# Optimization experiments

Measured on AMD Instinct MI355X. Metric: run time of the kernel, lower is better.

## Reference

```python
import jax, jax.numpy as jnp
import numpy as np
from jax import lax

NUM_EXPERTS = 256
TOP_K = 8
HIDDEN = 7168
N_GROUP = 8
TOPK_GROUP = 4
SCALING = 2.5
NORM_TOPK = True
EPG = NUM_EXPERTS // N_GROUP  # experts per group = 32


def setup_inputs() -> dict:
    key = jax.random.key(0)
    k1, k2, k3 = jax.random.split(key, 3)
    hidden_states = jax.random.normal(k1, (4, 2048, HIDDEN), dtype=jnp.float32)
    weight = jax.random.normal(k2, (NUM_EXPERTS, HIDDEN), dtype=jnp.float32) * 0.02
    e_score_correction_bias = jax.random.normal(k3, (NUM_EXPERTS,), dtype=jnp.float32) * 0.1
    return {"hidden_states": hidden_states, "weight": weight,
            "e_score_correction_bias": e_score_correction_bias}


def reference(hidden_states, weight, e_score_correction_bias):
    x = hidden_states.reshape(-1, hidden_states.shape[-1]).astype(jnp.float32)  # [T, H]
    router_logits = jnp.einsum('th,eh->te', x, weight.astype(jnp.float32))       # [T, E]
    scores = jax.nn.sigmoid(router_logits)
    scores_for_choice = scores + e_score_correction_bias[None, :]
    grouped = scores_for_choice.reshape(-1, N_GROUP, EPG)                        # [T, G, epg]
    group_scores = grouped.sum(axis=-1)                                          # [T, G]
    _, group_idx = lax.top_k(group_scores, TOPK_GROUP)                            # [T, kg]
    selected = jnp.take_along_axis(grouped, group_idx[:, :, None], axis=1)        # [T, kg, epg]
    flat = selected.reshape(-1, TOPK_GROUP * EPG)                                 # [T, kg*epg]
    _, flat_idx = lax.top_k(flat, TOP_K)                                          # [T, K]
    group_ord = flat_idx // EPG
    within = flat_idx % EPG
    actual_group = jnp.take_along_axis(group_idx, group_ord, axis=1)
    topk_indices = actual_group * EPG + within                                    # [T, K]
    topk_weights = jnp.take_along_axis(scores, topk_indices, axis=1)              # [T, K]
    if NORM_TOPK:
        topk_weights = topk_weights / (topk_weights.sum(axis=-1, keepdims=True) + 1e-20)
    topk_weights = topk_weights * SCALING
    return topk_indices, topk_weights
```

## Files before the change

### kernel.cpp

```cpp
#include <hip/hip_runtime.h>
#include <float.h>
#include <math.h>

#define NUM_T 8192
#define NUM_E 256
#define HID   7168

typedef __attribute__((ext_vector_type(16))) float f32x16;
typedef __attribute__((ext_vector_type(4))) _Float16 f16x4;
typedef __attribute__((ext_vector_type(8))) _Float16 f16x8;

#define MFMA(a, b, c) __builtin_amdgcn_mfma_f32_32x32x16_f16(a, b, c, 0, 0, 0)

__device__ __forceinline__ int lds_off(int row, int c8) {
  return (row << 6) + ((c8 ^ (row & 15)) << 2);
}

__device__ __forceinline__ void cvt4(float4 v, f16x4& h, f16x4& l) {
  h[0] = (_Float16)v.x; h[1] = (_Float16)v.y;
  h[2] = (_Float16)v.z; h[3] = (_Float16)v.w;
  l[0] = (_Float16)(v.x - (float)h[0]);
  l[1] = (_Float16)(v.y - (float)h[1]);
  l[2] = (_Float16)(v.z - (float)h[2]);
  l[3] = (_Float16)(v.w - (float)h[3]);
}

__device__ __forceinline__ f16x8 frag(const _Float16* buf, int row, int c8) {
  const f16x4 p0 = *reinterpret_cast<const f16x4*>(buf + lds_off(row, c8));
  const f16x4 p1 = *reinterpret_cast<const f16x4*>(buf + lds_off(row, c8 + 1));
  return __builtin_shufflevector(p0, p1, 0, 1, 2, 3, 4, 5, 6, 7);
}

template <int S>
__global__ __launch_bounds__(512, 2) void router_gemm_mfma(
    const float* __restrict__ X, const float* __restrict__ W,
    float* __restrict__ partial) {
  __shared__ _Float16 smem[2][384 * 64];

  const int tid = threadIdx.x;
  const int bid = blockIdx.x;
  int bx, by;
  if (S == 4) {
    const int xcd = bid & 7;
    by = xcd >> 1;
    bx = (bid >> 3) * 2 + (xcd & 1);
  } else if (S == 2) {
    const int xcd = bid & 7;
    by = xcd >> 2;
    bx = (bid >> 3) * 4 + (xcd & 3);
  } else {
    by = 0;
    bx = bid;
  }

  const int kLen = HID / S;
  const int nch = kLen / 32;
  const int t0 = bx * 128;
  const int k0 = by * kLen;

  const int xr = tid >> 2, xq = tid & 3;
  const int wr = tid >> 1, wq = tid & 1;
  const float* Xp = X + (size_t)(t0 + xr) * HID + k0 + xq * 8;
  const float* Wp = W + (size_t)wr * HID + k0 + wq * 16;

  int xo[4], wo[8];
  xo[0] = lds_off(xr, xq * 2);
  xo[1] = lds_off(xr, xq * 2 + 1);
  xo[2] = lds_off(xr, 8 + xq * 2);
  xo[3] = lds_off(xr, 8 + xq * 2 + 1);
#pragma unroll
  for (int j = 0; j < 4; ++j) {
    wo[j] = lds_off(128 + wr, wq * 4 + j);
    wo[4 + j] = lds_off(128 + wr, 8 + wq * 4 + j);
  }

  const int l = tid & 63, wave = tid >> 6;
  const int wm = wave >> 2, wn = wave & 3;
  const int la = l & 31, kh = l >> 5;
  const int ar0 = wm * 64 + la;
  const int br0 = 128 + wn * 64 + la;

  f32x16 acc[2][2];
#pragma unroll
  for (int i = 0; i < 2; ++i)
#pragma unroll
    for (int j = 0; j < 2; ++j)
#pragma unroll
      for (int r = 0; r < 16; ++r) acc[i][j][r] = 0.f;

  float4 xv[2], wv[4];

#define LOADC()                                            \
  do {                                                     \
    xv[0] = *reinterpret_cast<const float4*>(Xp);          \
    xv[1] = *reinterpret_cast<const float4*>(Xp + 4);      \
    wv[0] = *reinterpret_cast<const float4*>(Wp);          \
    wv[1] = *reinterpret_cast<const float4*>(Wp + 4);      \
    wv[2] = *reinterpret_cast<const float4*>(Wp + 8);      \
    wv[3] = *reinterpret_cast<const float4*>(Wp + 12);     \
    Xp += 32;                                              \
    Wp += 32;                                              \
  } while (0)

#define STAGE(dst)                                         \
  do {                                                     \
    f16x4 h_, l_;                                          \
    cvt4(xv[0], h_, l_);                                   \
    *reinterpret_cast<f16x4*>((dst) + xo[0]) = h_;         \
    *reinterpret_cast<f16x4*>((dst) + xo[2]) = l_;         \
    cvt4(xv[1], h_, l_);                                   \
    *reinterpret_cast<f16x4*>((dst) + xo[1]) = h_;         \
    *reinterpret_cast<f16x4*>((dst) + xo[3]) = l_;         \
    _Pragma("unroll") for (int j = 0; j < 4; ++j) {        \
      cvt4(wv[j], h_, l_);                                 \
      *reinterpret_cast<f16x4*>((dst) + wo[j]) = h_;       \
      *reinterpret_cast<f16x4*>((dst) + wo[4 + j]) = l_;   \
    }                                                      \
  } while (0)

  LOADC();
  STAGE(&smem[0][0]);
  __syncthreads();

  int cur = 0;
  for (int c = 0; c < nch; ++c) {
    const bool more = (c + 1) < nch;
    if (more) LOADC();

    const _Float16* buf = &smem[cur][0];
#pragma unroll
    for (int ks = 0; ks < 2; ++ks) {
      const int cb = ks * 4 + kh * 2;
      f16x8 ah0 = frag(buf, ar0, cb);
      f16x8 ah1 = frag(buf, ar0 + 32, cb);
      f16x8 bh0 = frag(buf, br0, cb);
      f16x8 bh1 = frag(buf, br0 + 32, cb);
      f16x8 al0 = frag(buf, ar0, cb + 8);
      f16x8 al1 = frag(buf, ar0 + 32, cb + 8);
      f16x8 bl0 = frag(buf, br0, cb + 8);
      f16x8 bl1 = frag(buf, br0 + 32, cb + 8);
      acc[0][0] = MFMA(ah0, bh0, acc[0][0]);
      acc[0][1] = MFMA(ah0, bh1, acc[0][1]);
      acc[1][0] = MFMA(ah1, bh0, acc[1][0]);
      acc[1][1] = MFMA(ah1, bh1, acc[1][1]);
      acc[0][0] = MFMA(ah0, bl0, acc[0][0]);
      acc[0][1] = MFMA(ah0, bl1, acc[0][1]);
      acc[1][0] = MFMA(ah1, bl0, acc[1][0]);
      acc[1][1] = MFMA(ah1, bl1, acc[1][1]);
      acc[0][0] = MFMA(al0, bh0, acc[0][0]);
      acc[0][1] = MFMA(al0, bh1, acc[0][1]);
      acc[1][0] = MFMA(al1, bh0, acc[1][0]);
      acc[1][1] = MFMA(al1, bh1, acc[1][1]);
    }

    if (more) STAGE(&smem[cur ^ 1][0]);
    __syncthreads();
    cur ^= 1;
  }

  float* out = partial + (size_t)by * NUM_T * NUM_E;
#pragma unroll
  for (int ti = 0; ti < 2; ++ti)
#pragma unroll
    for (int tj = 0; tj < 2; ++tj) {
      const int col = wn * 64 + tj * 32 + la;
      const int rb = t0 + wm * 64 + ti * 32 + 4 * kh;
#pragma unroll
      for (int r = 0; r < 16; ++r) {
        const int row = rb + (r & 3) + 8 * (r >> 2);
        out[(size_t)row * NUM_E + col] = acc[ti][tj][r];
      }
    }
#undef LOADC
#undef STAGE
}

__global__ __launch_bounds__(256) void router_select(
    const float* __restrict__ partial, int splitk,
    const float* __restrict__ bias, float* __restrict__ outIdx,
    float* __restrict__ outW) {
  const int lane = threadIdx.x & 63;
  const int t = blockIdx.x * 4 + (threadIdx.x >> 6);

  float lg[4] = {0.f, 0.f, 0.f, 0.f};
  for (int s = 0; s < splitk; ++s) {
    const float4 p = *reinterpret_cast<const float4*>(
        partial + ((size_t)s * NUM_T + t) * NUM_E + lane * 4);
    lg[0] += p.x;
    lg[1] += p.y;
    lg[2] += p.z;
    lg[3] += p.w;
  }
  const float4 bv = *reinterpret_cast<const float4*>(bias + lane * 4);

  float sc[4], bs[4];
#pragma unroll
  for (int j = 0; j < 4; ++j) {
    sc[j] = 1.0f / (1.0f + expf(-lg[j]));
  }
  bs[0] = sc[0] + bv.x;
  bs[1] = sc[1] + bv.y;
  bs[2] = sc[2] + bv.z;
  bs[3] = sc[3] + bv.w;

  const int myg = lane >> 3;
  float gsum = bs[0] + bs[1] + bs[2] + bs[3];
#pragma unroll
  for (int d = 1; d < 8; d <<= 1) gsum += __shfl_xor(gsum, d);

  float gsv[8];
#pragma unroll
  for (int g = 0; g < 8; ++g) gsv[g] = __shfl(gsum, g * 8);

  unsigned selm = 0;
  int myrank = 0;
#pragma unroll
  for (int r = 0; r < 4; ++r) {
    int best = -1;
    float bvv = -FLT_MAX;
#pragma unroll
    for (int g = 0; g < 8; ++g) {
      if (!((selm >> g) & 1u) && gsv[g] > bvv) {
        bvv = gsv[g];
        best = g;
      }
    }
    selm |= 1u << best;
    if (best == myg) myrank = r;
  }
  const bool gsel = ((selm >> myg) & 1u) != 0u;

  float myv[4];
#pragma unroll
  for (int j = 0; j < 4; ++j) myv[j] = gsel ? bs[j] : -FLT_MAX;

  const int ebase = lane << 2;
  const int flatb = myrank * 32 + (lane & 7) * 4;

  float chosen_s = 0.f;
  int ex_out = 0;
  float ssum = 0.f;
  for (int r = 0; r < 8; ++r) {
    float v = -FLT_MAX;
    int fl = 1 << 30;
    int ex = 0;
    float s = 0.f;
#pragma unroll
    for (int j = 0; j < 4; ++j) {
      const bool better = (myv[j] > v) || (myv[j] == v && (flatb + j) < fl);
      if (better) {
        v = myv[j];
        fl = flatb + j;
        ex = ebase + j;
        s = sc[j];
      }
    }
#pragma unroll
    for (int d = 32; d > 0; d >>= 1) {
      const float v2 = __shfl_xor(v, d);
      const int fl2 = __shfl_xor(fl, d);
      const int ex2 = __shfl_xor(ex, d);
      const float s2 = __shfl_xor(s, d);
      if (v2 > v || (v2 == v && fl2 < fl)) {
        v = v2;
        fl = fl2;
        ex = ex2;
        s = s2;
      }
    }
    ssum += s;
    if (lane == r) {
      chosen_s = s;
      ex_out = ex;
    }
    if ((ex >> 2) == lane) myv[ex & 3] = -FLT_MAX;
  }

  if (lane < 8) {
    outIdx[t * 8 + lane] = (float)ex_out;
    outW[t * 8 + lane] = chosen_s / (ssum + 1e-20f) * 2.5f;
  }
}

extern "C" void kernel_launch(void* const* d_in, const int* in_sizes, int n_in,
                              void* d_out, int out_size, void* d_ws,
                              size_t ws_size, hipStream_t stream) {
  const float* X = (const float*)d_in[0];
  const float* W = (const float*)d_in[1];
  const float* bias = (const float*)d_in[2];
  float* partial = (float*)d_ws;

  const size_t slice = (size_t)NUM_T * NUM_E * sizeof(float);
  int S;
  if (ws_size >= 4 * slice)
    S = 4;
  else if (ws_size >= 2 * slice)
    S = 2;
  else
    S = 1;

  if (S == 4)
    router_gemm_mfma<4><<<dim3(64 * 4), dim3(512), 0, stream>>>(X, W, partial);
  else if (S == 2)
    router_gemm_mfma<2><<<dim3(64 * 2), dim3(512), 0, stream>>>(X, W, partial);
  else
    router_gemm_mfma<1><<<dim3(64), dim3(512), 0, stream>>>(X, W, partial);

  float* outIdx = (float*)d_out;
  float* outW = outIdx + NUM_T * 8;
  router_select<<<NUM_T / 4, 256, 0, stream>>>(partial, S, bias, outIdx, outW);
}
```

Before: 441.7 us.

## Pad LDS rows, unroll main loop by two with deeper register prefetch

Replaces the XOR-swizzled LDS layout with padded rows of 136 bytes and precomputed byte pointers, which simplifies address arithmetic. The main loop is unrolled by two with two register staging sets, so global loads run two chunks ahead. __syncthreads is replaced with an explicit lgkmcnt wait plus s_barrier. The goal is to hide global load latency and cut index math, at the cost of extra VGPRs for the second staging set and possible bank conflicts from the padded layout. The loop now assumes an even chunk count.

```diff
diff --git a/kernel.cpp b/kernel.cpp
--- a/kernel.cpp
+++ b/kernel.cpp
@@ -6,15 +6,16 @@
 #define NUM_E 256
 #define HID   7168
 
+#define ROWB 136
+#define BUFB (384 * ROWB)
+
 typedef __attribute__((ext_vector_type(16))) float f32x16;
 typedef __attribute__((ext_vector_type(4))) _Float16 f16x4;
 typedef __attribute__((ext_vector_type(8))) _Float16 f16x8;
 
 #define MFMA(a, b, c) __builtin_amdgcn_mfma_f32_32x32x16_f16(a, b, c, 0, 0, 0)
 
-__device__ __forceinline__ int lds_off(int row, int c8) {
-  return (row << 6) + ((c8 ^ (row & 15)) << 2);
-}
+#define BARRIER() asm volatile("s_waitcnt lgkmcnt(0)\n\ts_barrier" ::: "memory")
 
 __device__ __forceinline__ void cvt4(float4 v, f16x4& h, f16x4& l) {
   h[0] = (_Float16)v.x; h[1] = (_Float16)v.y;
@@ -25,17 +26,21 @@
   l[3] = (_Float16)(v.w - (float)h[3]);
 }
 
-__device__ __forceinline__ f16x8 frag(const _Float16* buf, int row, int c8) {
-  const f16x4 p0 = *reinterpret_cast<const f16x4*>(buf + lds_off(row, c8));
-  const f16x4 p1 = *reinterpret_cast<const f16x4*>(buf + lds_off(row, c8 + 1));
-  return __builtin_shufflevector(p0, p1, 0, 1, 2, 3, 4, 5, 6, 7);
-}
+__device__ __forceinline__ f16x8 fr(const char* p, int off) {
+  const f16x4 a = *reinterpret_cast<const f16x4*>(p + off);
+  const f16x4 b = *reinterpret_cast<const f16x4*>(p + off + 8);
+  return __builtin_shufflevector(a, b, 0, 1, 2, 3, 4, 5, 6, 7);
+}
+
+struct Q {
+  float4 x0, x1, w0, w1, w2, w3;
+};
 
 template <int S>
 __global__ __launch_bounds__(512, 2) void router_gemm_mfma(
     const float* __restrict__ X, const float* __restrict__ W,
     float* __restrict__ partial) {
-  __shared__ _Float16 smem[2][384 * 64];
+  __shared__ __align__(16) char lds[2 * BUFB];
 
   const int tid = threadIdx.x;
   const int bid = blockIdx.x;
@@ -62,23 +67,14 @@
   const int wr = tid >> 1, wq = tid & 1;
   const float* Xp = X + (size_t)(t0 + xr) * HID + k0 + xq * 8;
   const float* Wp = W + (size_t)wr * HID + k0 + wq * 16;
-
-  int xo[4], wo[8];
-  xo[0] = lds_off(xr, xq * 2);
-  xo[1] = lds_off(xr, xq * 2 + 1);
-  xo[2] = lds_off(xr, 8 + xq * 2);
-  xo[3] = lds_off(xr, 8 + xq * 2 + 1);
-#pragma unroll
-  for (int j = 0; j < 4; ++j) {
-    wo[j] = lds_off(128 + wr, wq * 4 + j);
-    wo[4 + j] = lds_off(128 + wr, 8 + wq * 4 + j);
-  }
+  char* wx = lds + xr * ROWB + xq * 16;
+  char* ww = lds + (128 + wr) * ROWB + wq * 32;
 
   const int l = tid & 63, wave = tid >> 6;
   const int wm = wave >> 2, wn = wave & 3;
   const int la = l & 31, kh = l >> 5;
-  const int ar0 = wm * 64 + la;
-  const int br0 = 128 + wn * 64 + la;
+  const char* ra = lds + (wm * 64 + la) * ROWB + kh * 16;
+  const char* rb = lds + (128 + wn * 64 + la) * ROWB + kh * 16;
 
   f32x16 acc[2][2];
 #pragma unroll
@@ -88,74 +84,83 @@
 #pragma unroll
       for (int r = 0; r < 16; ++r) acc[i][j][r] = 0.f;
 
-  float4 xv[2], wv[4];
-
-#define LOADC()                                            \
-  do {                                                     \
-    xv[0] = *reinterpret_cast<const float4*>(Xp);          \
-    xv[1] = *reinterpret_cast<const float4*>(Xp + 4);      \
-    wv[0] = *reinterpret_cast<const float4*>(Wp);          \
-    wv[1] = *reinterpret_cast<const float4*>(Wp + 4);      \
-    wv[2] = *reinterpret_cast<const float4*>(Wp + 8);      \
-    wv[3] = *reinterpret_cast<const float4*>(Wp + 12);     \
-    Xp += 32;                                              \
-    Wp += 32;                                              \
+#define LOADC(q)                                   \
+  do {                                             \
+    q.x0 = *reinterpret_cast<const float4*>(Xp);   \
+    q.x1 = *reinterpret_cast<const float4*>(Xp + 4); \
+    q.w0 = *reinterpret_cast<const float4*>(Wp);   \
+    q.w1 = *reinterpret_cast<const float4*>(Wp + 4); \
+    q.w2 = *reinterpret_cast<const float4*>(Wp + 8); \
+    q.w3 = *reinterpret_cast<const float4*>(Wp + 12); \
+    Xp += 32;                                      \
+    Wp += 32;                                      \
   } while (0)
 
-#define STAGE(dst)                                         \
-  do {                                                     \
-    f16x4 h_, l_;                                          \
-    cvt4(xv[0], h_, l_);                                   \
-    *reinterpret_cast<f16x4*>((dst) + xo[0]) = h_;         \
-    *reinterpret_cast<f16x4*>((dst) + xo[2]) = l_;         \
-    cvt4(xv[1], h_, l_);                                   \
-    *reinterpret_cast<f16x4*>((dst) + xo[1]) = h_;         \
-    *reinterpret_cast<f16x4*>((dst) + xo[3]) = l_;         \
-    _Pragma("unroll") for (int j = 0; j < 4; ++j) {        \
-      cvt4(wv[j], h_, l_);                                 \
-      *reinterpret_cast<f16x4*>((dst) + wo[j]) = h_;       \
-      *reinterpret_cast<f16x4*>((dst) + wo[4 + j]) = l_;   \
-    }                                                      \
+#define STAGE(B, q)                                            \
+  do {                                                         \
+    f16x4 h_, l_;                                              \
+    cvt4(q.x0, h_, l_);                                        \
+    *reinterpret_cast<f16x4*>(wx + (B) + 0) = h_;              \
+    *reinterpret_cast<f16x4*>(wx + (B) + 64) = l_;             \
+    cvt4(q.x1, h_, l_);                                        \
+    *reinterpret_cast<f16x4*>(wx + (B) + 8) = h_;              \
+    *reinterpret_cast<f16x4*>(wx + (B) + 72) = l_;             \
+    cvt4(q.w0, h_, l_);                                        \
+    *reinterpret_cast<f16x4*>(ww + (B) + 0) = h_;              \
+    *reinterpret_cast<f16x4*>(ww + (B) + 64) = l_;             \
+    cvt4(q.w1, h_, l_);                                        \
+    *reinterpret_cast<f16x4*>(ww + (B) + 8) = h_;              \
+    *reinterpret_cast<f16x4*>(ww + (B) + 72) = l_;             \
+    cvt4(q.w2, h_, l_);                                        \
+    *reinterpret_cast<f16x4*>(ww + (B) + 16) = h_;             \
+    *reinterpret_cast<f16x4*>(ww + (B) + 80) = l_;             \
+    cvt4(q.w3, h_, l_);                                        \
+    *reinterpret_cast<f16x4*>(ww + (B) + 24) = h_;             \
+    *reinterpret_cast<f16x4*>(ww + (B) + 88) = l_;             \
   } while (0)
 
-  LOADC();
-  STAGE(&smem[0][0]);
-  __syncthreads();
-
-  int cur = 0;
-  for (int c = 0; c < nch; ++c) {
-    const bool more = (c + 1) < nch;
-    if (more) LOADC();
-
-    const _Float16* buf = &smem[cur][0];
-#pragma unroll
-    for (int ks = 0; ks < 2; ++ks) {
-      const int cb = ks * 4 + kh * 2;
-      f16x8 ah0 = frag(buf, ar0, cb);
-      f16x8 ah1 = frag(buf, ar0 + 32, cb);
-      f16x8 bh0 = frag(buf, br0, cb);
-      f16x8 bh1 = frag(buf, br0 + 32, cb);
-      f16x8 al0 = frag(buf, ar0, cb + 8);
-      f16x8 al1 = frag(buf, ar0 + 32, cb + 8);
-      f16x8 bl0 = frag(buf, br0, cb + 8);
-      f16x8 bl1 = frag(buf, br0 + 32, cb + 8);
-      acc[0][0] = MFMA(ah0, bh0, acc[0][0]);
-      acc[0][1] = MFMA(ah0, bh1, acc[0][1]);
-      acc[1][0] = MFMA(ah1, bh0, acc[1][0]);
-      acc[1][1] = MFMA(ah1, bh1, acc[1][1]);
-      acc[0][0] = MFMA(ah0, bl0, acc[0][0]);
-      acc[0][1] = MFMA(ah0, bl1, acc[0][1]);
-      acc[1][0] = MFMA(ah1, bl0, acc[1][0]);
-      acc[1][1] = MFMA(ah1, bl1, acc[1][1]);
-      acc[0][0] = MFMA(al0, bh0, acc[0][0]);
-      acc[0][1] = MFMA(al0, bh1, acc[0][1]);
-      acc[1][0] = MFMA(al1, bh0, acc[1][0]);
-      acc[1][1] = MFMA(al1, bh1, acc[1][1]);
-    }
-
-    if (more) STAGE(&smem[cur ^ 1][0]);
-    __syncthreads();
-    cur ^= 1;
+#define MF_PHASE(B)                                            \
+  do {                                                         \
+    _Pragma("unroll") for (int ks = 0; ks < 2; ++ks) {         \
+      const int o = (B) + ks * 32;                             \
+      f16x8 ah0 = fr(ra, o);                                   \
+      f16x8 ah1 = fr(ra, o + 32 * ROWB);                       \
+      f16x8 bh0 = fr(rb, o);                                   \
+      f16x8 bh1 = fr(rb, o + 32 * ROWB);                       \
+      f16x8 al0 = fr(ra, o + 64);                              \
+      f16x8 al1 = fr(ra, o + 64 + 32 * ROWB);                  \
+      f16x8 bl0 = fr(rb, o + 64);                              \
+      f16x8 bl1 = fr(rb, o + 64 + 32 * ROWB);                  \
+      acc[0][0] = MFMA(ah0, bh0, acc[0][0]);                   \
+      acc[0][1] = MFMA(ah0, bh1, acc[0][1]);                   \
+      acc[1][0] = MFMA(ah1, bh0, acc[1][0]);                   \
+      acc[1][1] = MFMA(ah1, bh1, acc[1][1]);                   \
+      acc[0][0] = MFMA(ah0, bl0, acc[0][0]);                   \
+      acc[0][1] = MFMA(ah0, bl1, acc[0][1]);                   \
+      acc[1][0] = MFMA(ah1, bl0, acc[1][0]);                   \
+      acc[1][1] = MFMA(ah1, bl1, acc[1][1]);                   \
+      acc[0][0] = MFMA(al0, bh0, acc[0][0]);                   \
+      acc[0][1] = MFMA(al0, bh1, acc[0][1]);                   \
+      acc[1][0] = MFMA(al1, bh0, acc[1][0]);                   \
+      acc[1][1] = MFMA(al1, bh1, acc[1][1]);                   \
+    }                                                          \
+  } while (0)
+
+  Q q0, q1;
+  LOADC(q0);
+  LOADC(q1);
+  STAGE(0, q0);
+  BARRIER();
+
+  for (int c = 0; c < nch; c += 2) {
+    if (c + 2 < nch) LOADC(q0);
+    MF_PHASE(0);
+    STAGE(BUFB, q1);
+    BARRIER();
+    if (c + 3 < nch) LOADC(q1);
+    MF_PHASE(BUFB);
+    if (c + 2 < nch) STAGE(0, q0);
+    BARRIER();
   }
 
   float* out = partial + (size_t)by * NUM_T * NUM_E;
@@ -164,15 +169,16 @@
 #pragma unroll
     for (int tj = 0; tj < 2; ++tj) {
       const int col = wn * 64 + tj * 32 + la;
-      const int rb = t0 + wm * 64 + ti * 32 + 4 * kh;
+      const int rbse = t0 + wm * 64 + ti * 32 + 4 * kh;
 #pragma unroll
       for (int r = 0; r < 16; ++r) {
-        const int row = rb + (r & 3) + 8 * (r >> 2);
+        const int row = rbse + (r & 3) + 8 * (r >> 2);
         out[(size_t)row * NUM_E + col] = acc[ti][tj][r];
       }
     }
 #undef LOADC
 #undef STAGE
+#undef MF_PHASE
 }
 
 __global__ __launch_bounds__(256) void router_select(
```

New measurement: 387.5 us. 1.14x faster.
